# Kernel tuning notes

Measured on AMD Instinct MI355X. Metric: run time of the kernel, lower is better.

Reference implementation:

```python
import jax, jax.numpy as jnp
import numpy as np

B, IN, H = 4096, 1024, 1024

def setup_inputs() -> dict:
    key = jax.random.key(0)
    ks = jax.random.split(key, 7)
    s_in = 1.0 / np.sqrt(IN)
    s_h = 1.0 / np.sqrt(H)
    return {
        "x": jax.random.normal(ks[0], (B, IN), dtype=jnp.float32),
        "h": jax.random.normal(ks[1], (B, H), dtype=jnp.float32),
        "W_ih": jax.random.uniform(ks[2], (3 * H, IN), jnp.float32, -s_in, s_in),
        "b_ih": jax.random.uniform(ks[3], (3 * H,), jnp.float32, -s_in, s_in),
        "W_rzh": jax.random.uniform(ks[4], (2 * H, H), jnp.float32, -s_h, s_h),
        "W_nh": jax.random.uniform(ks[5], (H, H), jnp.float32, -s_h, s_h),
        "b_nh": jax.random.uniform(ks[6], (H,), jnp.float32, -s_h, s_h),
    }


def reference(x, h, W_ih, b_ih, W_rzh, W_nh, b_nh):
    # Input projection: one fused matmul producing (B, 3H)
    x_proj = x @ W_ih.T + b_ih
    r_x, z_x, n_x = jnp.split(x_proj, 3, axis=-1)
    # Fused r/z hidden projection (B, 2H)
    rz_h = h @ W_rzh.T
    r_h, z_h = jnp.split(rz_h, 2, axis=-1)
    r = jax.nn.sigmoid(r_x + r_h)
    z = jax.nn.sigmoid(z_x + z_h)
    n = jnp.tanh(n_x + r * (h @ W_nh.T + b_nh))
    return (1.0 - z) * n + z * h
```

## Files before the change

kernel.cpp:

```cpp
#include <hip/hip_runtime.h>
#include <hip/hip_bf16.h>
#include <stdint.h>


typedef __attribute__((ext_vector_type(8))) short bfrag8;
typedef __attribute__((ext_vector_type(16))) float f32x16;

__device__ __forceinline__ unsigned short f2bf(float f) {
  union { float f; unsigned u; } v; v.f = f;
  unsigned u = v.u;
  return (unsigned short)((u + 0x7fffu + ((u >> 16) & 1u)) >> 16);
}

__device__ __forceinline__ void load_lds16(const void* g, void* l) {
  __builtin_amdgcn_global_load_lds(
      (const __attribute__((address_space(1))) void*)g,
      (__attribute__((address_space(3))) void*)l, 16, 0, 0);
}

__device__ __forceinline__ void cvt8(const float* __restrict__ src,
                                     unsigned short* __restrict__ dst) {
  float4 f0 = ((const float4*)src)[0];
  float4 f1 = ((const float4*)src)[1];
  uint4 o;
  o.x = (unsigned)f2bf(f0.x) | ((unsigned)f2bf(f0.y) << 16);
  o.y = (unsigned)f2bf(f0.z) | ((unsigned)f2bf(f0.w) << 16);
  o.z = (unsigned)f2bf(f1.x) | ((unsigned)f2bf(f1.y) << 16);
  o.w = (unsigned)f2bf(f1.z) | ((unsigned)f2bf(f1.w) << 16);
  *(uint4*)dst = o;
}

__global__ void prep_all(const float* __restrict__ x, const float* __restrict__ h,
                         const float* __restrict__ W_ih, const float* __restrict__ W_rzh,
                         const float* __restrict__ W_nh,
                         unsigned short* __restrict__ A2t, unsigned short* __restrict__ Wbt) {
  int idx = blockIdx.x * blockDim.x + threadIdx.x;
  if (idx < (1 << 20)) {
    int L = idx & 63;
    int kc = (idx >> 6) & 63;
    int win = (idx >> 12) & 1;
    int T = idx >> 13;
    int row = T * 32 + (L & 31);
    int col = kc * 16 + (L >> 5) * 8;
    const float* src = (win ? h : x) + (size_t)row * 1024 + col;
    cvt8(src, A2t + (size_t)idx * 8);
  } else {
    int c2 = idx - (1 << 20);
    int L = c2 & 63;
    int kc = (c2 >> 6) & 63;
    int rest = c2 >> 12;
    int bn = rest / 6;
    int item = rest - bn * 6;
    int jc = bn * 32 + (L & 31);
    int col = kc * 16 + (L >> 5) * 8;
    const float* src;
    switch (item) {
      case 0:  src = W_ih  + (size_t)jc * 1024 + col; break;
      case 1:  src = W_ih  + (size_t)(1024 + jc) * 1024 + col; break;
      case 2:  src = W_ih  + (size_t)(2048 + jc) * 1024 + col; break;
      case 3:  src = W_rzh + (size_t)jc * 1024 + col; break;
      case 4:  src = W_rzh + (size_t)(1024 + jc) * 1024 + col; break;
      default: src = W_nh  + (size_t)jc * 1024 + col; break;
    }
    cvt8(src, Wbt + (size_t)c2 * 8);
  }
}

__global__ __launch_bounds__(256, 2)
void gru_gemm_fused(const unsigned short* __restrict__ A2t,
                    const unsigned short* __restrict__ Wbt,
                    const float* __restrict__ h,
                    const float* __restrict__ b_ih,
                    const float* __restrict__ b_nh,
                    float* __restrict__ out) {
  __shared__ unsigned short ldsA[8 * 2 * 2 * 512];
  __shared__ unsigned short ldsB[6 * 2 * 512];

  const int lane = threadIdx.x & 63;
  const int wave = threadIdx.x >> 6;
  const int row0 = blockIdx.x << 8;
  const int bn = blockIdx.y;

  const int wm = wave << 6;
  const int m32 = lane & 31;
  const int khalf = lane >> 5;

  const unsigned short* gA[2][2][2];
  unsigned short* lA[2][2][2];
#pragma unroll
  for (int t = 0; t < 2; ++t)
#pragma unroll
    for (int win = 0; win < 2; ++win)
#pragma unroll
      for (int kcl = 0; kcl < 2; ++kcl) {
        int T = blockIdx.x * 8 + wave * 2 + t;
        gA[t][win][kcl] = A2t + (size_t)(T * 2 + win) * 32768 + kcl * 512 + lane * 8;
        lA[t][win][kcl] = &ldsA[(((wave * 2 + t) * 2 + win) * 2 + kcl) * 512];
      }

  const unsigned short* gB[3];
  unsigned short* lB[3];
#pragma unroll
  for (int i = 0; i < 3; ++i) {
    int j = wave * 3 + i;
    int item = j >> 1;
    int kcl = j & 1;
    gB[i] = Wbt + (size_t)(bn * 6 + item) * 32768 + kcl * 512 + lane * 8;
    lB[i] = &ldsB[(item * 2 + kcl) * 512];
  }

  f32x16 acc[2][4] = {};

  for (int k0 = 0; k0 < 1024; k0 += 32) {
    const size_t koff = (size_t)k0 * 32;
    __syncthreads();
#pragma unroll
    for (int t = 0; t < 2; ++t)
#pragma unroll
      for (int win = 0; win < 2; ++win)
#pragma unroll
        for (int kcl = 0; kcl < 2; ++kcl)
          load_lds16(gA[t][win][kcl] + koff, lA[t][win][kcl]);
#pragma unroll
    for (int i = 0; i < 3; ++i) load_lds16(gB[i] + koff, lB[i]);
    __syncthreads();

#pragma unroll
    for (int ks = 0; ks < 2; ++ks) {
      const int fo = ks * 512 + lane * 8;
      bfrag8 a0[2], a1[2], bfr[6];
#pragma unroll
      for (int t = 0; t < 2; ++t) {
        a0[t] = *(const bfrag8*)&ldsA[((wave * 2 + t) * 2 + 0) * 1024 + fo];
        a1[t] = *(const bfrag8*)&ldsA[((wave * 2 + t) * 2 + 1) * 1024 + fo];
      }
#pragma unroll
      for (int it = 0; it < 6; ++it)
        bfr[it] = *(const bfrag8*)&ldsB[it * 1024 + fo];

#pragma unroll
      for (int t = 0; t < 2; ++t) {
        acc[t][0] = __builtin_amdgcn_mfma_f32_32x32x16_bf16(a0[t], bfr[0], acc[t][0], 0, 0, 0);
        acc[t][0] = __builtin_amdgcn_mfma_f32_32x32x16_bf16(a1[t], bfr[3], acc[t][0], 0, 0, 0);
        acc[t][1] = __builtin_amdgcn_mfma_f32_32x32x16_bf16(a0[t], bfr[1], acc[t][1], 0, 0, 0);
        acc[t][1] = __builtin_amdgcn_mfma_f32_32x32x16_bf16(a1[t], bfr[4], acc[t][1], 0, 0, 0);
        acc[t][2] = __builtin_amdgcn_mfma_f32_32x32x16_bf16(a0[t], bfr[2], acc[t][2], 0, 0, 0);
        acc[t][3] = __builtin_amdgcn_mfma_f32_32x32x16_bf16(a1[t], bfr[5], acc[t][3], 0, 0, 0);
      }
    }
  }

  const int jcol = bn * 32 + m32;
  const float br  = b_ih[jcol];
  const float bz  = b_ih[1024 + jcol];
  const float bnv = b_ih[2048 + jcol];
  const float bh  = b_nh[jcol];

#pragma unroll
  for (int t = 0; t < 2; ++t) {
#pragma unroll
    for (int i = 0; i < 16; ++i) {
      int mrow = row0 + wm + t * 32 + (i & 3) + ((i >> 2) << 3) + (khalf << 2);
      size_t off = (size_t)mrow * 1024 + jcol;
      float rg = 1.f / (1.f + __expf(-(acc[t][0][i] + br)));
      float zg = 1.f / (1.f + __expf(-(acc[t][1][i] + bz)));
      float e2 = __expf(2.f * (acc[t][2][i] + bnv + rg * (acc[t][3][i] + bh)));
      float ng = 1.f - 2.f / (e2 + 1.f);
      float hv = h[off];
      out[off] = ng + zg * (hv - ng);
    }
  }
}

extern "C" void kernel_launch(void* const* d_in, const int* in_sizes, int n_in,
                              void* d_out, int out_size, void* d_ws, size_t ws_size,
                              hipStream_t stream) {
  const float* x     = (const float*)d_in[0];
  const float* h     = (const float*)d_in[1];
  const float* W_ih  = (const float*)d_in[2];
  const float* b_ih  = (const float*)d_in[3];
  const float* W_rzh = (const float*)d_in[4];
  const float* W_nh  = (const float*)d_in[5];
  const float* b_nh  = (const float*)d_in[6];
  float* out = (float*)d_out;

  unsigned short* A2t = (unsigned short*)d_ws;
  unsigned short* Wbt = A2t + (size_t)(1 << 20) * 8;

  prep_all<<<dim3(7168), dim3(256), 0, stream>>>(x, h, W_ih, W_rzh, W_nh, A2t, Wbt);
  gru_gemm_fused<<<dim3(16, 32), dim3(256), 0, stream>>>(A2t, Wbt, h, b_ih, b_nh, out);
}
```

Before: 164.3 us.

## Double-buffer LDS and widen block to 512 threads covering two column tiles

The GEMM kernel now uses 8 waves per block, each block covering 256 rows by two 32-column tiles, so A tiles are shared across twice the output columns. LDS is double-buffered with one k-chunk of 16 per step: the next chunk's global-to-LDS loads are issued before computing on the current buffer, removing one barrier per step. Loading is specialised, with four waves fetching A and four fetching B. This trades more barriers (64 iterations instead of 32) and higher LDS use per block for better A reuse and load/compute overlap.

Measured after the change: 178.3 us. 1.09x slower.

```diff
diff --git a/kernel.cpp b/kernel.cpp
--- a/kernel.cpp
+++ b/kernel.cpp
@@ -66,91 +66,101 @@
   }
 }
 
-__global__ __launch_bounds__(256, 2)
+__global__ __launch_bounds__(512, 2)
 void gru_gemm_fused(const unsigned short* __restrict__ A2t,
                     const unsigned short* __restrict__ Wbt,
                     const float* __restrict__ h,
                     const float* __restrict__ b_ih,
                     const float* __restrict__ b_nh,
                     float* __restrict__ out) {
-  __shared__ unsigned short ldsA[8 * 2 * 2 * 512];
-  __shared__ unsigned short ldsB[6 * 2 * 512];
+  __shared__ unsigned short ldsA[2][16 * 512];
+  __shared__ unsigned short ldsB[2][12 * 512];
 
   const int lane = threadIdx.x & 63;
   const int wave = threadIdx.x >> 6;
-  const int row0 = blockIdx.x << 8;
-  const int bn = blockIdx.y;
-
-  const int wm = wave << 6;
+  const int half = wave & 1;
+  const int wq = wave >> 1;
   const int m32 = lane & 31;
   const int khalf = lane >> 5;
-
-  const unsigned short* gA[2][2][2];
-  unsigned short* lA[2][2][2];
-#pragma unroll
-  for (int t = 0; t < 2; ++t)
-#pragma unroll
-    for (int win = 0; win < 2; ++win)
-#pragma unroll
-      for (int kcl = 0; kcl < 2; ++kcl) {
-        int T = blockIdx.x * 8 + wave * 2 + t;
-        gA[t][win][kcl] = A2t + (size_t)(T * 2 + win) * 32768 + kcl * 512 + lane * 8;
-        lA[t][win][kcl] = &ldsA[(((wave * 2 + t) * 2 + win) * 2 + kcl) * 512];
+  const int row0 = blockIdx.x << 8;
+  const int bn2 = blockIdx.y;
+
+  const unsigned short* gsrc[4];
+  int ldst[4];
+  int nreg;
+  bool isA = (wave < 4);
+  if (isA) {
+    nreg = 4;
+#pragma unroll
+    for (int i = 0; i < 4; ++i) {
+      int idx = wave * 4 + i;
+      int Tloc = idx >> 1;
+      int win = idx & 1;
+      int T = blockIdx.x * 8 + Tloc;
+      gsrc[i] = A2t + (size_t)(T * 2 + win) * 32768 + lane * 8;
+      ldst[i] = idx * 512;
+    }
+  } else {
+    nreg = 3;
+#pragma unroll
+    for (int i = 0; i < 3; ++i) {
+      int idx = (wave - 4) * 3 + i;
+      int bh = idx >= 6;
+      int item = idx - bh * 6;
+      int bn_eff = bn2 * 2 + bh;
+      gsrc[i] = Wbt + (size_t)(bn_eff * 6 + item) * 32768 + lane * 8;
+      ldst[i] = idx * 512;
+    }
+  }
+
+  if (isA) {
+#pragma unroll
+    for (int i = 0; i < 4; ++i) load_lds16(gsrc[i], &ldsA[0][ldst[i]]);
+  } else {
+#pragma unroll
+    for (int i = 0; i < 3; ++i) load_lds16(gsrc[i], &ldsB[0][ldst[i]]);
+  }
+
+  f32x16 acc[2][4] = {};
+  const int fo = lane * 8;
+
+  for (int it = 0; it < 64; ++it) {
+    const int buf = it & 1;
+    __syncthreads();
+    if (it < 63) {
+      const size_t koff = (size_t)(it + 1) * 512;
+      const int nb = buf ^ 1;
+      if (isA) {
+#pragma unroll
+        for (int i = 0; i < 4; ++i) load_lds16(gsrc[i] + koff, &ldsA[nb][ldst[i]]);
+      } else {
+#pragma unroll
+        for (int i = 0; i < 3; ++i) load_lds16(gsrc[i] + koff, &ldsB[nb][ldst[i]]);
       }
-
-  const unsigned short* gB[3];
-  unsigned short* lB[3];
-#pragma unroll
-  for (int i = 0; i < 3; ++i) {
-    int j = wave * 3 + i;
-    int item = j >> 1;
-    int kcl = j & 1;
-    gB[i] = Wbt + (size_t)(bn * 6 + item) * 32768 + kcl * 512 + lane * 8;
-    lB[i] = &ldsB[(item * 2 + kcl) * 512];
-  }
-
-  f32x16 acc[2][4] = {};
-
-  for (int k0 = 0; k0 < 1024; k0 += 32) {
-    const size_t koff = (size_t)k0 * 32;
-    __syncthreads();
-#pragma unroll
-    for (int t = 0; t < 2; ++t)
-#pragma unroll
-      for (int win = 0; win < 2; ++win)
-#pragma unroll
-        for (int kcl = 0; kcl < 2; ++kcl)
-          load_lds16(gA[t][win][kcl] + koff, lA[t][win][kcl]);
-#pragma unroll
-    for (int i = 0; i < 3; ++i) load_lds16(gB[i] + koff, lB[i]);
-    __syncthreads();
-
-#pragma unroll
-    for (int ks = 0; ks < 2; ++ks) {
-      const int fo = ks * 512 + lane * 8;
-      bfrag8 a0[2], a1[2], bfr[6];
-#pragma unroll
-      for (int t = 0; t < 2; ++t) {
-        a0[t] = *(const bfrag8*)&ldsA[((wave * 2 + t) * 2 + 0) * 1024 + fo];
-        a1[t] = *(const bfrag8*)&ldsA[((wave * 2 + t) * 2 + 1) * 1024 + fo];
-      }
-#pragma unroll
-      for (int it = 0; it < 6; ++it)
-        bfr[it] = *(const bfrag8*)&ldsB[it * 1024 + fo];
-
-#pragma unroll
-      for (int t = 0; t < 2; ++t) {
-        acc[t][0] = __builtin_amdgcn_mfma_f32_32x32x16_bf16(a0[t], bfr[0], acc[t][0], 0, 0, 0);
-        acc[t][0] = __builtin_amdgcn_mfma_f32_32x32x16_bf16(a1[t], bfr[3], acc[t][0], 0, 0, 0);
-        acc[t][1] = __builtin_amdgcn_mfma_f32_32x32x16_bf16(a0[t], bfr[1], acc[t][1], 0, 0, 0);
-        acc[t][1] = __builtin_amdgcn_mfma_f32_32x32x16_bf16(a1[t], bfr[4], acc[t][1], 0, 0, 0);
-        acc[t][2] = __builtin_amdgcn_mfma_f32_32x32x16_bf16(a0[t], bfr[2], acc[t][2], 0, 0, 0);
-        acc[t][3] = __builtin_amdgcn_mfma_f32_32x32x16_bf16(a1[t], bfr[5], acc[t][3], 0, 0, 0);
-      }
-    }
-  }
-
-  const int jcol = bn * 32 + m32;
+    }
+
+    bfrag8 a0[2], a1[2], bfr[6];
+#pragma unroll
+    for (int t = 0; t < 2; ++t) {
+      a0[t] = *(const bfrag8*)&ldsA[buf][((wq * 2 + t) * 2 + 0) * 512 + fo];
+      a1[t] = *(const bfrag8*)&ldsA[buf][((wq * 2 + t) * 2 + 1) * 512 + fo];
+    }
+#pragma unroll
+    for (int i6 = 0; i6 < 6; ++i6)
+      bfr[i6] = *(const bfrag8*)&ldsB[buf][(half * 6 + i6) * 512 + fo];
+
+#pragma unroll
+    for (int t = 0; t < 2; ++t) {
+      acc[t][0] = __builtin_amdgcn_mfma_f32_32x32x16_bf16(a0[t], bfr[0], acc[t][0], 0, 0, 0);
+      acc[t][0] = __builtin_amdgcn_mfma_f32_32x32x16_bf16(a1[t], bfr[3], acc[t][0], 0, 0, 0);
+      acc[t][1] = __builtin_amdgcn_mfma_f32_32x32x16_bf16(a0[t], bfr[1], acc[t][1], 0, 0, 0);
+      acc[t][1] = __builtin_amdgcn_mfma_f32_32x32x16_bf16(a1[t], bfr[4], acc[t][1], 0, 0, 0);
+      acc[t][2] = __builtin_amdgcn_mfma_f32_32x32x16_bf16(a0[t], bfr[2], acc[t][2], 0, 0, 0);
+      acc[t][3] = __builtin_amdgcn_mfma_f32_32x32x16_bf16(a1[t], bfr[5], acc[t][3], 0, 0, 0);
+    }
+  }
+
+  const int jcol = (bn2 * 2 + half) * 32 + m32;
   const float br  = b_ih[jcol];
   const float bz  = b_ih[1024 + jcol];
   const float bnv = b_ih[2048 + jcol];
@@ -160,7 +170,7 @@
   for (int t = 0; t < 2; ++t) {
 #pragma unroll
     for (int i = 0; i < 16; ++i) {
-      int mrow = row0 + wm + t * 32 + (i & 3) + ((i >> 2) << 3) + (khalf << 2);
+      int mrow = row0 + wq * 64 + t * 32 + (i & 3) + ((i >> 2) << 3) + (khalf << 2);
       size_t off = (size_t)mrow * 1024 + jcol;
       float rg = 1.f / (1.f + __expf(-(acc[t][0][i] + br)));
       float zg = 1.f / (1.f + __expf(-(acc[t][1][i] + bz)));
@@ -188,5 +198,5 @@
   unsigned short* Wbt = A2t + (size_t)(1 << 20) * 8;
 
   prep_all<<<dim3(7168), dim3(256), 0, stream>>>(x, h, W_ih, W_rzh, W_nh, A2t, Wbt);
-  gru_gemm_fused<<<dim3(16, 32), dim3(256), 0, stream>>>(A2t, Wbt, h, b_ih, b_nh, out);
-}
+  gru_gemm_fused<<<dim3(16, 16), dim3(512), 0, stream>>>(A2t, Wbt, h, b_ih, b_nh, out);
+}
```

## Replace LDS-staged GEMM with direct-to-register double-buffered fragment loads

Applied to the files above, without the earlier changes.

Drops the shared-memory staging of pre-swizzled bf16 A and B fragments. Each wave now loads its MFMA operands straight from global memory into registers, double-buffered across k-chunks. The block shape changes to 512 threads covering a 128-row by 4-column-block tile, so that waves sharing data can hit in cache, and a periodic barrier keeps the waves loosely in step. The aim is to remove LDS round-trips and the per-iteration barriers. The cost is more global and L2 traffic, because operands are no longer shared through LDS, plus higher register pressure.

Measured after the change: 175.5 us. 1.07x slower.

```diff
diff --git a/kernel.cpp b/kernel.cpp
--- a/kernel.cpp
+++ b/kernel.cpp
@@ -10,12 +10,6 @@
   union { float f; unsigned u; } v; v.f = f;
   unsigned u = v.u;
   return (unsigned short)((u + 0x7fffu + ((u >> 16) & 1u)) >> 16);
-}
-
-__device__ __forceinline__ void load_lds16(const void* g, void* l) {
-  __builtin_amdgcn_global_load_lds(
-      (const __attribute__((address_space(1))) void*)g,
-      (__attribute__((address_space(3))) void*)l, 16, 0, 0);
 }
 
 __device__ __forceinline__ void cvt8(const float* __restrict__ src,
@@ -66,88 +60,75 @@
   }
 }
 
-__global__ __launch_bounds__(256, 2)
-void gru_gemm_fused(const unsigned short* __restrict__ A2t,
-                    const unsigned short* __restrict__ Wbt,
-                    const float* __restrict__ h,
-                    const float* __restrict__ b_ih,
-                    const float* __restrict__ b_nh,
-                    float* __restrict__ out) {
-  __shared__ unsigned short ldsA[8 * 2 * 2 * 512];
-  __shared__ unsigned short ldsB[6 * 2 * 512];
+__device__ __forceinline__ void mfma_body(f32x16 acc[2][4],
+                                          const bfrag8 fa[4], const bfrag8 fb[6]) {
+#pragma unroll
+  for (int t = 0; t < 2; ++t) {
+    acc[t][0] = __builtin_amdgcn_mfma_f32_32x32x16_bf16(fa[t * 2 + 0], fb[0], acc[t][0], 0, 0, 0);
+    acc[t][0] = __builtin_amdgcn_mfma_f32_32x32x16_bf16(fa[t * 2 + 1], fb[3], acc[t][0], 0, 0, 0);
+    acc[t][1] = __builtin_amdgcn_mfma_f32_32x32x16_bf16(fa[t * 2 + 0], fb[1], acc[t][1], 0, 0, 0);
+    acc[t][1] = __builtin_amdgcn_mfma_f32_32x32x16_bf16(fa[t * 2 + 1], fb[4], acc[t][1], 0, 0, 0);
+    acc[t][2] = __builtin_amdgcn_mfma_f32_32x32x16_bf16(fa[t * 2 + 0], fb[2], acc[t][2], 0, 0, 0);
+    acc[t][3] = __builtin_amdgcn_mfma_f32_32x32x16_bf16(fa[t * 2 + 1], fb[5], acc[t][3], 0, 0, 0);
+  }
+}
 
+__global__ __launch_bounds__(512, 2)
+void gru_gemm_reg(const unsigned short* __restrict__ A2t,
+                  const unsigned short* __restrict__ Wbt,
+                  const float* __restrict__ h,
+                  const float* __restrict__ b_ih,
+                  const float* __restrict__ b_nh,
+                  float* __restrict__ out) {
   const int lane = threadIdx.x & 63;
   const int wave = threadIdx.x >> 6;
-  const int row0 = blockIdx.x << 8;
-  const int bn = blockIdx.y;
-
-  const int wm = wave << 6;
+  const int mw = wave >> 2;
+  const int bnl = wave & 3;
+  const int mg = blockIdx.x >> 3;
+  const int bng = blockIdx.x & 7;
+  const int bn = bng * 4 + bnl;
+  const int Tbase = mg * 4 + mw * 2;
   const int m32 = lane & 31;
   const int khalf = lane >> 5;
 
-  const unsigned short* gA[2][2][2];
-  unsigned short* lA[2][2][2];
+  const unsigned short* ga[4];
 #pragma unroll
   for (int t = 0; t < 2; ++t)
 #pragma unroll
     for (int win = 0; win < 2; ++win)
+      ga[t * 2 + win] = A2t + (size_t)((Tbase + t) * 2 + win) * 32768 + lane * 8;
+  const unsigned short* gb[6];
 #pragma unroll
-      for (int kcl = 0; kcl < 2; ++kcl) {
-        int T = blockIdx.x * 8 + wave * 2 + t;
-        gA[t][win][kcl] = A2t + (size_t)(T * 2 + win) * 32768 + kcl * 512 + lane * 8;
-        lA[t][win][kcl] = &ldsA[(((wave * 2 + t) * 2 + win) * 2 + kcl) * 512];
-      }
-
-  const unsigned short* gB[3];
-  unsigned short* lB[3];
-#pragma unroll
-  for (int i = 0; i < 3; ++i) {
-    int j = wave * 3 + i;
-    int item = j >> 1;
-    int kcl = j & 1;
-    gB[i] = Wbt + (size_t)(bn * 6 + item) * 32768 + kcl * 512 + lane * 8;
-    lB[i] = &ldsB[(item * 2 + kcl) * 512];
-  }
+  for (int it = 0; it < 6; ++it)
+    gb[it] = Wbt + (size_t)(bn * 6 + it) * 32768 + lane * 8;
 
   f32x16 acc[2][4] = {};
 
-  for (int k0 = 0; k0 < 1024; k0 += 32) {
-    const size_t koff = (size_t)k0 * 32;
-    __syncthreads();
+  bfrag8 fa0[4], fb0[6], fa1[4], fb1[6];
 #pragma unroll
-    for (int t = 0; t < 2; ++t)
+  for (int i = 0; i < 4; ++i) fa0[i] = *(const bfrag8*)ga[i];
 #pragma unroll
-      for (int win = 0; win < 2; ++win)
+  for (int i = 0; i < 6; ++i) fb0[i] = *(const bfrag8*)gb[i];
+
+  for (int kc2 = 0; kc2 < 64; kc2 += 2) {
+    if ((kc2 & 3) == 0) __syncthreads();
+    {
+      const int off = (kc2 + 1) * 512;
 #pragma unroll
-        for (int kcl = 0; kcl < 2; ++kcl)
-          load_lds16(gA[t][win][kcl] + koff, lA[t][win][kcl]);
+      for (int i = 0; i < 4; ++i) fa1[i] = *(const bfrag8*)(ga[i] + off);
 #pragma unroll
-    for (int i = 0; i < 3; ++i) load_lds16(gB[i] + koff, lB[i]);
-    __syncthreads();
+      for (int i = 0; i < 6; ++i) fb1[i] = *(const bfrag8*)(gb[i] + off);
+    }
+    mfma_body(acc, fa0, fb0);
 
+    if (kc2 < 62) {
+      const int off = (kc2 + 2) * 512;
 #pragma unroll
-    for (int ks = 0; ks < 2; ++ks) {
-      const int fo = ks * 512 + lane * 8;
-      bfrag8 a0[2], a1[2], bfr[6];
+      for (int i = 0; i < 4; ++i) fa0[i] = *(const bfrag8*)(ga[i] + off);
 #pragma unroll
-      for (int t = 0; t < 2; ++t) {
-        a0[t] = *(const bfrag8*)&ldsA[((wave * 2 + t) * 2 + 0) * 1024 + fo];
-        a1[t] = *(const bfrag8*)&ldsA[((wave * 2 + t) * 2 + 1) * 1024 + fo];
-      }
-#pragma unroll
-      for (int it = 0; it < 6; ++it)
-        bfr[it] = *(const bfrag8*)&ldsB[it * 1024 + fo];
-
-#pragma unroll
-      for (int t = 0; t < 2; ++t) {
-        acc[t][0] = __builtin_amdgcn_mfma_f32_32x32x16_bf16(a0[t], bfr[0], acc[t][0], 0, 0, 0);
-        acc[t][0] = __builtin_amdgcn_mfma_f32_32x32x16_bf16(a1[t], bfr[3], acc[t][0], 0, 0, 0);
-        acc[t][1] = __builtin_amdgcn_mfma_f32_32x32x16_bf16(a0[t], bfr[1], acc[t][1], 0, 0, 0);
-        acc[t][1] = __builtin_amdgcn_mfma_f32_32x32x16_bf16(a1[t], bfr[4], acc[t][1], 0, 0, 0);
-        acc[t][2] = __builtin_amdgcn_mfma_f32_32x32x16_bf16(a0[t], bfr[2], acc[t][2], 0, 0, 0);
-        acc[t][3] = __builtin_amdgcn_mfma_f32_32x32x16_bf16(a1[t], bfr[5], acc[t][3], 0, 0, 0);
-      }
+      for (int i = 0; i < 6; ++i) fb0[i] = *(const bfrag8*)(gb[i] + off);
     }
+    mfma_body(acc, fa1, fb1);
   }
 
   const int jcol = bn * 32 + m32;
@@ -160,7 +141,7 @@
   for (int t = 0; t < 2; ++t) {
 #pragma unroll
     for (int i = 0; i < 16; ++i) {
-      int mrow = row0 + wm + t * 32 + (i & 3) + ((i >> 2) << 3) + (khalf << 2);
+      int mrow = mg * 128 + mw * 64 + t * 32 + (i & 3) + ((i >> 2) << 3) + (khalf << 2);
       size_t off = (size_t)mrow * 1024 + jcol;
       float rg = 1.f / (1.f + __expf(-(acc[t][0][i] + br)));
       float zg = 1.f / (1.f + __expf(-(acc[t][1][i] + bz)));
@@ -188,5 +169,5 @@
   unsigned short* Wbt = A2t + (size_t)(1 << 20) * 8;
 
   prep_all<<<dim3(7168), dim3(256), 0, stream>>>(x, h, W_ih, W_rzh, W_nh, A2t, Wbt);
-  gru_gemm_fused<<<dim3(16, 32), dim3(256), 0, stream>>>(A2t, Wbt, h, b_ih, b_nh, out);
+  gru_gemm_reg<<<dim3(256), dim3(512), 0, stream>>>(A2t, Wbt, h, b_ih, b_nh, out);
 }
```

## Prefetch next K-tile into registers while computing current tile from LDS

Applied to the files above, without the earlier changes.

Replaces direct global-to-LDS loads with register staging: each thread loads the next K slice of A and B fragments into registers while MFMAs consume the current slice in shared memory, then writes them to LDS at the start of the next iteration. The goal is to overlap global memory latency with compute instead of stalling at the barrier after each load. The cost is extra VGPRs for the 11 staged fragments, which may pressure occupancy at two blocks per CU, plus an added barrier per iteration.

Measured after the change: 167.4 us. About the same (+1.9%).

```diff
diff --git a/kernel.cpp b/kernel.cpp
--- a/kernel.cpp
+++ b/kernel.cpp
@@ -10,12 +10,6 @@
   union { float f; unsigned u; } v; v.f = f;
   unsigned u = v.u;
   return (unsigned short)((u + 0x7fffu + ((u >> 16) & 1u)) >> 16);
-}
-
-__device__ __forceinline__ void load_lds16(const void* g, void* l) {
-  __builtin_amdgcn_global_load_lds(
-      (const __attribute__((address_space(1))) void*)g,
-      (__attribute__((address_space(3))) void*)l, 16, 0, 0);
 }
 
 __device__ __forceinline__ void cvt8(const float* __restrict__ src,
@@ -67,76 +61,71 @@
 }
 
 __global__ __launch_bounds__(256, 2)
-void gru_gemm_fused(const unsigned short* __restrict__ A2t,
-                    const unsigned short* __restrict__ Wbt,
-                    const float* __restrict__ h,
-                    const float* __restrict__ b_ih,
-                    const float* __restrict__ b_nh,
-                    float* __restrict__ out) {
-  __shared__ unsigned short ldsA[8 * 2 * 2 * 512];
-  __shared__ unsigned short ldsB[6 * 2 * 512];
+void gru_gemm_pipe(const unsigned short* __restrict__ A2t,
+                   const unsigned short* __restrict__ Wbt,
+                   const float* __restrict__ h,
+                   const float* __restrict__ b_ih,
+                   const float* __restrict__ b_nh,
+                   float* __restrict__ out) {
+  __shared__ unsigned short lds[44 * 512];
 
   const int lane = threadIdx.x & 63;
   const int wave = threadIdx.x >> 6;
-  const int row0 = blockIdx.x << 8;
+  const int mg = blockIdx.x;
   const int bn = blockIdx.y;
-
-  const int wm = wave << 6;
+  const int row0 = mg << 8;
   const int m32 = lane & 31;
   const int khalf = lane >> 5;
 
-  const unsigned short* gA[2][2][2];
-  unsigned short* lA[2][2][2];
+  const unsigned short* gsrc[11];
+  int ldst[11];
 #pragma unroll
-  for (int t = 0; t < 2; ++t)
-#pragma unroll
-    for (int win = 0; win < 2; ++win)
-#pragma unroll
-      for (int kcl = 0; kcl < 2; ++kcl) {
-        int T = blockIdx.x * 8 + wave * 2 + t;
-        gA[t][win][kcl] = A2t + (size_t)(T * 2 + win) * 32768 + kcl * 512 + lane * 8;
-        lA[t][win][kcl] = &ldsA[(((wave * 2 + t) * 2 + win) * 2 + kcl) * 512];
-      }
-
-  const unsigned short* gB[3];
-  unsigned short* lB[3];
-#pragma unroll
-  for (int i = 0; i < 3; ++i) {
-    int j = wave * 3 + i;
-    int item = j >> 1;
-    int kcl = j & 1;
-    gB[i] = Wbt + (size_t)(bn * 6 + item) * 32768 + kcl * 512 + lane * 8;
-    lB[i] = &ldsB[(item * 2 + kcl) * 512];
+  for (int i = 0; i < 11; ++i) {
+    int c = wave * 11 + i;
+    ldst[i] = c * 512 + lane * 8;
+    if (c < 32) {
+      int Tloc = c >> 2;
+      int win = (c >> 1) & 1;
+      int kcl = c & 1;
+      gsrc[i] = A2t + ((size_t)((mg * 8 + Tloc) * 2 + win) * 64 + kcl) * 512 + lane * 8;
+    } else {
+      int d = c - 32;
+      int item = d >> 1;
+      int kcl = d & 1;
+      gsrc[i] = Wbt + ((size_t)(bn * 6 + item) * 64 + kcl) * 512 + lane * 8;
+    }
   }
 
   f32x16 acc[2][4] = {};
+  const int fo = lane * 8;
 
-  for (int k0 = 0; k0 < 1024; k0 += 32) {
-    const size_t koff = (size_t)k0 * 32;
-    __syncthreads();
+  bfrag8 st[11];
 #pragma unroll
-    for (int t = 0; t < 2; ++t)
+  for (int i = 0; i < 11; ++i) st[i] = *(const bfrag8*)gsrc[i];
+
+  for (int it = 0; it < 32; ++it) {
 #pragma unroll
-      for (int win = 0; win < 2; ++win)
-#pragma unroll
-        for (int kcl = 0; kcl < 2; ++kcl)
-          load_lds16(gA[t][win][kcl] + koff, lA[t][win][kcl]);
-#pragma unroll
-    for (int i = 0; i < 3; ++i) load_lds16(gB[i] + koff, lB[i]);
+    for (int i = 0; i < 11; ++i) *(bfrag8*)&lds[ldst[i]] = st[i];
     __syncthreads();
 
+    if (it < 31) {
+      const size_t go = (size_t)(it + 1) * 1024;
 #pragma unroll
-    for (int ks = 0; ks < 2; ++ks) {
-      const int fo = ks * 512 + lane * 8;
+      for (int i = 0; i < 11; ++i) st[i] = *(const bfrag8*)(gsrc[i] + go);
+    }
+
+#pragma unroll
+    for (int kcl = 0; kcl < 2; ++kcl) {
       bfrag8 a0[2], a1[2], bfr[6];
 #pragma unroll
       for (int t = 0; t < 2; ++t) {
-        a0[t] = *(const bfrag8*)&ldsA[((wave * 2 + t) * 2 + 0) * 1024 + fo];
-        a1[t] = *(const bfrag8*)&ldsA[((wave * 2 + t) * 2 + 1) * 1024 + fo];
+        int Tloc = wave * 2 + t;
+        a0[t] = *(const bfrag8*)&lds[((Tloc * 2 + 0) * 2 + kcl) * 512 + fo];
+        a1[t] = *(const bfrag8*)&lds[((Tloc * 2 + 1) * 2 + kcl) * 512 + fo];
       }
 #pragma unroll
-      for (int it = 0; it < 6; ++it)
-        bfr[it] = *(const bfrag8*)&ldsB[it * 1024 + fo];
+      for (int i6 = 0; i6 < 6; ++i6)
+        bfr[i6] = *(const bfrag8*)&lds[(32 + i6 * 2 + kcl) * 512 + fo];
 
 #pragma unroll
       for (int t = 0; t < 2; ++t) {
@@ -148,6 +137,7 @@
         acc[t][3] = __builtin_amdgcn_mfma_f32_32x32x16_bf16(a1[t], bfr[5], acc[t][3], 0, 0, 0);
       }
     }
+    __syncthreads();
   }
 
   const int jcol = bn * 32 + m32;
@@ -160,7 +150,7 @@
   for (int t = 0; t < 2; ++t) {
 #pragma unroll
     for (int i = 0; i < 16; ++i) {
-      int mrow = row0 + wm + t * 32 + (i & 3) + ((i >> 2) << 3) + (khalf << 2);
+      int mrow = row0 + wave * 64 + t * 32 + (i & 3) + ((i >> 2) << 3) + (khalf << 2);
       size_t off = (size_t)mrow * 1024 + jcol;
       float rg = 1.f / (1.f + __expf(-(acc[t][0][i] + br)));
       float zg = 1.f / (1.f + __expf(-(acc[t][1][i] + bz)));
@@ -188,5 +178,5 @@
   unsigned short* Wbt = A2t + (size_t)(1 << 20) * 8;
 
   prep_all<<<dim3(7168), dim3(256), 0, stream>>>(x, h, W_ih, W_rzh, W_nh, A2t, Wbt);
-  gru_gemm_fused<<<dim3(16, 32), dim3(256), 0, stream>>>(A2t, Wbt, h, b_ih, b_nh, out);
+  gru_gemm_pipe<<<dim3(16, 32), dim3(256), 0, stream>>>(A2t, Wbt, h, b_ih, b_nh, out);
 }
```
